# Kernel optimization log

Measured on AMD Instinct MI355X. Metric: run time of the kernel, lower is better.

The kernel has to match this reference:

```python
import jax, jax.numpy as jnp
import numpy as np
from jax import lax

IMG_H, IMG_W = 800.0, 800.0
REG_WEIGHTS = (10.0, 10.0, 5.0, 5.0)
SCORE_THRESH = 0.05
NMS_THRESH = 0.5
NUM_DETECTIONS = 100
MIN_SIZE = 1.0
BBOX_XFORM_CLIP = float(np.log(1000.0 / 16.0))


def setup_inputs() -> dict:
    key = jax.random.key(0)
    k1, k2, k3, k4 = jax.random.split(key, 4)
    N, C = 1000, 81
    class_logit = jax.random.normal(k1, (N, C), dtype=jnp.float32) * 2.0
    box_regression = jax.random.normal(k2, (N, C * 4), dtype=jnp.float32)
    # proposals: valid (x1,y1,x2,y2) boxes inside the 800x800 image
    ctr = jax.random.uniform(k3, (N, 2), dtype=jnp.float32) * 800.0
    wh = jax.random.uniform(k4, (N, 2), dtype=jnp.float32) * 200.0 + 8.0
    x1y1 = jnp.clip(ctr - 0.5 * wh, 0.0, 800.0)
    x2y2 = jnp.clip(ctr + 0.5 * wh, 0.0, 800.0)
    proposal = jnp.concatenate([x1y1, x2y2], axis=1)
    return dict(class_logit=class_logit, box_regression=box_regression, proposal=proposal)


def decode_boxes(deltas, boxes):
    # deltas: [..., 4] (dx,dy,dw,dh); boxes: [..., 4] (x1,y1,x2,y2)
    wx, wy, ww, wh = REG_WEIGHTS
    widths = boxes[..., 2] - boxes[..., 0]
    heights = boxes[..., 3] - boxes[..., 1]
    ctr_x = boxes[..., 0] + 0.5 * widths
    ctr_y = boxes[..., 1] + 0.5 * heights
    dx = deltas[..., 0] / wx
    dy = deltas[..., 1] / wy
    dw = jnp.minimum(deltas[..., 2] / ww, BBOX_XFORM_CLIP)
    dh = jnp.minimum(deltas[..., 3] / wh, BBOX_XFORM_CLIP)
    pcx = dx * widths + ctr_x
    pcy = dy * heights + ctr_y
    pw = jnp.exp(dw) * widths
    ph = jnp.exp(dh) * heights
    return jnp.stack([pcx - 0.5 * pw, pcy - 0.5 * ph, pcx + 0.5 * pw, pcy + 0.5 * ph], axis=-1)


def pairwise_iou(b):
    # b: [N, 4] -> [N, N]
    area = (b[:, 2] - b[:, 0]) * (b[:, 3] - b[:, 1])
    lt = jnp.maximum(b[:, None, :2], b[None, :, :2])
    rb = jnp.minimum(b[:, None, 2:], b[None, :, 2:])
    wh = jnp.clip(rb - lt, 0.0)
    inter = wh[..., 0] * wh[..., 1]
    return inter / (area[:, None] + area[None, :] - inter + 1e-9)


def nms_one_class(boxes, scores):
    # boxes: [N, 4]; scores: [N] with invalid entries masked to -1.
    # Exact greedy NMS: sort by score desc, suppress IoU > NMS_THRESH.
    N = boxes.shape[0]
    order = jnp.argsort(-scores)
    b = boxes[order]
    s = scores[order]
    iou = pairwise_iou(b)
    valid = s > -0.5

    def body(carry, xs):
        keep, i = carry
        row, v = xs
        suppressed = jnp.any(keep & (row > NMS_THRESH))
        keep = keep.at[i].set(v & jnp.logical_not(suppressed))
        return (keep, i + 1), None

    (keep, _), _ = lax.scan(body, (jnp.zeros((N,), bool), jnp.int32(0)), (iou, valid))
    s_kept = jnp.where(keep, s, -1.0)
    top_s, top_i = lax.top_k(s_kept, NUM_DETECTIONS)  # kept are already score-sorted
    out_valid = top_s > -0.5
    out_boxes = jnp.where(out_valid[:, None], b[top_i], 0.0)
    out_scores = jnp.where(out_valid, top_s, 0.0)
    return out_boxes, out_scores, out_valid


def reference(class_logit, box_regression, proposal):
    N, C = class_logit.shape
    pred_score = jax.nn.softmax(class_logit, axis=-1)           # [N, C]
    deltas = box_regression.reshape(N, C, 4)
    boxes = decode_boxes(deltas[:, 1:, :], proposal[:, None, :])  # [N, C-1, 4]
    # clip to image (process_box)
    boxes = jnp.stack([
        jnp.clip(boxes[..., 0], 0.0, IMG_W),
        jnp.clip(boxes[..., 1], 0.0, IMG_H),
        jnp.clip(boxes[..., 2], 0.0, IMG_W),
        jnp.clip(boxes[..., 3], 0.0, IMG_H),
    ], axis=-1)
    w = boxes[..., 2] - boxes[..., 0]
    h = boxes[..., 3] - boxes[..., 1]
    score_fg = pred_score[:, 1:]                                 # [N, C-1]
    valid = (score_fg >= SCORE_THRESH) & (w >= MIN_SIZE) & (h >= MIN_SIZE)
    scores_m = jnp.where(valid, score_fg, -1.0)
    boxes_c = jnp.transpose(boxes, (1, 0, 2))                    # [C-1, N, 4]
    scores_c = scores_m.T                                        # [C-1, N]
    out_boxes, out_scores, out_valid = jax.vmap(nms_one_class)(boxes_c, scores_c)
    labels = jnp.broadcast_to(jnp.arange(1, C, dtype=jnp.int32)[:, None], out_scores.shape)
    labels = jnp.where(out_valid, labels, 0)
    # padded per-class detections: boxes [C-1, D, 4], scores/labels/valid [C-1, D]
    return out_boxes, out_scores, labels, out_valid
```

## Files before the change

kernel.cpp:

```cpp
#include <hip/hip_runtime.h>
#include <math.h>

#define N_PROP   1000
#define C_ALL    81
#define N_FG     80
#define TOPK     100
#define CAP      1024
#define IMG_WH   800.0f
#define SCORE_TH 0.05f
#define NMS_TH   0.5f
#define MIN_SZ   1.0f
#define BBOX_CLIP 4.135166556742356f

#define DEC_BLK  320
#define NMS_BLK  256

typedef unsigned long long u64;

#define WS_CNT_STRIDE 16
#define WS_KEYS_OFF   8192
#define WS_FLT_OFF    (WS_KEYS_OFF + N_FG * CAP * 8)
#define WS_REQUIRED   (WS_FLT_OFF + 5ull * N_FG * CAP * 4)

__global__ __launch_bounds__(DEC_BLK) void decode_kernel(
    const float* __restrict__ logits,
    const float* __restrict__ boxreg,
    const float* __restrict__ prop,
    char* __restrict__ ws)
{
    int*   cnt  = (int*)ws;
    u64*   wkey = (u64*)(ws + WS_KEYS_OFF);
    float* wx1  = (float*)(ws + WS_FLT_OFF);
    float* wy1  = wx1 + N_FG * CAP;
    float* wx2  = wy1 + N_FG * CAP;
    float* wy2  = wx2 + N_FG * CAP;
    float* war  = wy2 + N_FG * CAP;

    __shared__ float2 s_ms[4];

    const int b    = blockIdx.x;
    const int tid  = threadIdx.x;
    const int wave = tid >> 6;
    const int lane = tid & 63;

    if (wave < 4) {
        const float* row = logits + (4 * b + wave) * C_ALL;
        float v1 = row[lane];
        float v2 = (lane < C_ALL - 64) ? row[64 + lane] : 0.f;

        float m = (lane < C_ALL - 64) ? fmaxf(v1, v2) : v1;
        #pragma unroll
        for (int off = 32; off >= 1; off >>= 1)
            m = fmaxf(m, __shfl_xor(m, off, 64));

        float s = expf(v1 - m) + ((lane < C_ALL - 64) ? expf(v2 - m) : 0.0f);
        #pragma unroll
        for (int off = 32; off >= 1; off >>= 1)
            s += __shfl_xor(s, off, 64);

        if (lane == 0) s_ms[wave] = make_float2(m, s);
    }
    __syncthreads();

    const int r   = tid / N_FG;
    const int cc  = tid - r * N_FG;
    const int n   = 4 * b + r;
    const int col = cc + 1;

    float2 ms = s_ms[r];
    float score = expf(logits[n * C_ALL + col] - ms.x) / ms.y;

    float4 p = *(const float4*)(prop + n * 4);
    float w  = p.z - p.x;
    float h  = p.w - p.y;
    float pcx0 = p.x + 0.5f * w;
    float pcy0 = p.y + 0.5f * h;

    float4 d = *(const float4*)(boxreg + n * (C_ALL * 4) + col * 4);
    float dx = d.x / 10.0f;
    float dy = d.y / 10.0f;
    float dw = fminf(d.z / 5.0f, BBOX_CLIP);
    float dh = fminf(d.w / 5.0f, BBOX_CLIP);

    float pcx = dx * w + pcx0;
    float pcy = dy * h + pcy0;
    float pw  = expf(dw) * w;
    float ph  = expf(dh) * h;

    float x1 = fminf(fmaxf(pcx - 0.5f * pw, 0.0f), IMG_WH);
    float y1 = fminf(fmaxf(pcy - 0.5f * ph, 0.0f), IMG_WH);
    float x2 = fminf(fmaxf(pcx + 0.5f * pw, 0.0f), IMG_WH);
    float y2 = fminf(fmaxf(pcy + 0.5f * ph, 0.0f), IMG_WH);

    float bw = x2 - x1;
    float bh = y2 - y1;
    if (score >= SCORE_TH && bw >= MIN_SZ && bh >= MIN_SZ) {
        int slot = atomicAdd(&cnt[cc * WS_CNT_STRIDE], 1);
        unsigned int fb = __float_as_uint(score);
        int base = cc * CAP + slot;
        wkey[base] = ((u64)fb << 10) | (u64)(1023 - n);
        wx1[base] = x1; wy1[base] = y1; wx2[base] = x2; wy2[base] = y2;
        war[base] = bw * bh;
    }
}

__global__ __launch_bounds__(NMS_BLK) void nms_kernel(
    const char* __restrict__ ws,
    float* __restrict__ out)
{
    const int*   cnt  = (const int*)ws;
    const u64*   wkey = (const u64*)(ws + WS_KEYS_OFF);
    const float* wx1  = (const float*)(ws + WS_FLT_OFF);
    const float* wy1  = wx1 + N_FG * CAP;
    const float* wx2  = wy1 + N_FG * CAP;
    const float* wy2  = wx2 + N_FG * CAP;
    const float* war  = wy2 + N_FG * CAP;

    __shared__ u64   s_key[CAP];
    __shared__ float cx1[CAP], cy1[CAP], cx2[CAP], cy2[CAP], car[CAP];
    __shared__ u64   s_skey[CAP];
    __shared__ float sx1[CAP], sy1[CAP], sx2[CAP], sy2[CAP], sar[CAP];
    __shared__ u64   s_mask[256 * 4];
    __shared__ u64   s_keep[4];
    __shared__ unsigned char s_rem[CAP];
    __shared__ int   s_emit;

    const int c   = blockIdx.x;
    const int tid = threadIdx.x;
    const int col = c + 1;

    const int OFF_SCORES = N_FG * TOPK * 4;
    const int OFF_LABELS = OFF_SCORES + N_FG * TOPK;
    const int OFF_VALID  = OFF_LABELS + N_FG * TOPK;

    if (tid < 175) {
        float4 z = make_float4(0.f, 0.f, 0.f, 0.f);
        if (tid < 100)      ((float4*)(out + c * TOPK * 4))[tid] = z;
        else if (tid < 125) ((float4*)(out + OFF_SCORES + c * TOPK))[tid - 100] = z;
        else if (tid < 150) ((float4*)(out + OFF_LABELS + c * TOPK))[tid - 125] = z;
        else                ((float4*)(out + OFF_VALID  + c * TOPK))[tid - 150] = z;
    }
    if (tid == 0) s_emit = 0;

    const int V = cnt[c * WS_CNT_STRIDE];
    if (V == 0) return;

    for (int t = tid; t < V; t += NMS_BLK) {
        int base = c * CAP + t;
        s_key[t] = wkey[base];
        cx1[t] = wx1[base]; cy1[t] = wy1[base];
        cx2[t] = wx2[base]; cy2[t] = wy2[base];
        car[t] = war[base];
    }
    __syncthreads();

    for (int t = tid; t < V; t += NMS_BLK) {
        u64 myk = s_key[t];
        int rank = 0;
        #pragma unroll 4
        for (int j = 0; j < V; ++j) rank += (s_key[j] > myk) ? 1 : 0;
        s_skey[rank] = myk;
        sx1[rank] = cx1[t]; sy1[rank] = cy1[t];
        sx2[rank] = cx2[t]; sy2[rank] = cy2[t];
        sar[rank] = car[t];
    }
    __syncthreads();

    if (V <= 64) {
        if (tid < 64) {
            const int lane = tid;
            bool act = lane < V;
            float bx1 = 0.f, by1 = 0.f, bx2 = 0.f, by2 = 0.f, bar = 0.f;
            if (act) {
                bx1 = sx1[lane]; by1 = sy1[lane];
                bx2 = sx2[lane]; by2 = sy2[lane];
                bar = sar[lane];
            }
            u64 myrow = 0;
            for (int i = 0; i < V; ++i) {
                float ix1 = __shfl(bx1, i, 64);
                float iy1 = __shfl(by1, i, 64);
                float ix2 = __shfl(bx2, i, 64);
                float iy2 = __shfl(by2, i, 64);
                float iar = __shfl(bar, i, 64);
                float lx = fmaxf(ix1, bx1);
                float ly = fmaxf(iy1, by1);
                float rx = fminf(ix2, bx2);
                float ry = fminf(iy2, by2);
                float iw = fmaxf(rx - lx, 0.0f);
                float ih = fmaxf(ry - ly, 0.0f);
                float inter = iw * ih;
                float iou = inter / (iar + bar - inter + 1e-9f);
                u64 bal = __ballot(act && (iou > NMS_TH));
                if (lane == i) {
                    u64 upper = (i == 63) ? 0ull : ~((1ull << (i + 1)) - 1ull);
                    myrow = bal & upper;
                }
            }
            u64 S = 0, K = 0;
            for (int i = 0; i < V; ++i) {
                if (!((S >> i) & 1ull)) {
                    K |= 1ull << i;
                    S |= __shfl(myrow, i, 64);
                }
            }
            if (act && ((K >> lane) & 1ull)) {
                int rank = __popcll(K & ((1ull << lane) - 1ull));
                float score = __uint_as_float((unsigned int)(s_skey[lane] >> 10));
                out[(c * TOPK + rank) * 4 + 0] = bx1;
                out[(c * TOPK + rank) * 4 + 1] = by1;
                out[(c * TOPK + rank) * 4 + 2] = bx2;
                out[(c * TOPK + rank) * 4 + 3] = by2;
                out[OFF_SCORES + c * TOPK + rank] = score;
                out[OFF_LABELS + c * TOPK + rank] = (float)col;
                out[OFF_VALID  + c * TOPK + rank] = 1.0f;
            }
        }
    } else if (V <= 256) {
        for (int i = tid; i < V; i += NMS_BLK) {
            float x1i = sx1[i], y1i = sy1[i], x2i = sx2[i], y2i = sy2[i];
            float ai  = sar[i];
            for (int w = 0; w < 4; ++w) {
                u64 mrow = 0;
                int j0 = w << 6;
                int j1 = min(V, j0 + 64);
                for (int j = max(j0, i + 1); j < j1; ++j) {
                    float lx = fmaxf(x1i, sx1[j]);
                    float ly = fmaxf(y1i, sy1[j]);
                    float rx = fminf(x2i, sx2[j]);
                    float ry = fminf(y2i, sy2[j]);
                    float iw = fmaxf(rx - lx, 0.0f);
                    float ih = fmaxf(ry - ly, 0.0f);
                    float inter = iw * ih;
                    float iou = inter / (ai + sar[j] - inter + 1e-9f);
                    if (iou > NMS_TH) mrow |= 1ull << (j - j0);
                }
                s_mask[(i << 2) + w] = mrow;
            }
        }
        __syncthreads();

        if (tid == 0) {
            u64 r0 = 0, r1 = 0, r2 = 0, r3 = 0;
            u64 k0 = 0, k1 = 0, k2 = 0, k3 = 0;
            int kept = 0;
            u64 p0 = s_mask[0], p1 = s_mask[1], p2 = s_mask[2], p3 = s_mask[3];
            u64 q0 = 0, q1 = 0, q2 = 0, q3 = 0;
            if (V > 1) {
                const u64* nr = &s_mask[4];
                q0 = nr[0]; q1 = nr[1]; q2 = nr[2]; q3 = nr[3];
            }
            for (int i = 0; i < V; ++i) {
                u64 t0 = 0, t1 = 0, t2 = 0, t3 = 0;
                if (i + 2 < V) {
                    const u64* nr = &s_mask[(i + 2) << 2];
                    t0 = nr[0]; t1 = nr[1]; t2 = nr[2]; t3 = nr[3];
                }
                int w = i >> 6;
                u64 bit = 1ull << (i & 63);
                u64 rw = (w == 0) ? r0 : (w == 1) ? r1 : (w == 2) ? r2 : r3;
                if (!(rw & bit)) {
                    if (w == 0) k0 |= bit; else if (w == 1) k1 |= bit;
                    else if (w == 2) k2 |= bit; else k3 |= bit;
                    if (++kept >= TOPK) break;
                    r0 |= p0; r1 |= p1; r2 |= p2; r3 |= p3;
                }
                p0 = q0; p1 = q1; p2 = q2; p3 = q3;
                q0 = t0; q1 = t1; q2 = t2; q3 = t3;
            }
            s_keep[0] = k0; s_keep[1] = k1; s_keep[2] = k2; s_keep[3] = k3;
        }
        __syncthreads();

        u64 kw0 = s_keep[0], kw1 = s_keep[1], kw2 = s_keep[2], kw3 = s_keep[3];
        for (int t = tid; t < V; t += NMS_BLK) {
            int w = t >> 6;
            u64 kw = (w == 0) ? kw0 : (w == 1) ? kw1 : (w == 2) ? kw2 : kw3;
            if (!((kw >> (t & 63)) & 1ull)) continue;
            int rank = 0;
            if (w > 0) rank += __popcll(kw0);
            if (w > 1) rank += __popcll(kw1);
            if (w > 2) rank += __popcll(kw2);
            rank += __popcll(kw & ((1ull << (t & 63)) - 1ull));
            if (rank < TOPK) {
                float score = __uint_as_float((unsigned int)(s_skey[t] >> 10));
                out[(c * TOPK + rank) * 4 + 0] = sx1[t];
                out[(c * TOPK + rank) * 4 + 1] = sy1[t];
                out[(c * TOPK + rank) * 4 + 2] = sx2[t];
                out[(c * TOPK + rank) * 4 + 3] = sy2[t];
                out[OFF_SCORES + c * TOPK + rank] = score;
                out[OFF_LABELS + c * TOPK + rank] = (float)col;
                out[OFF_VALID  + c * TOPK + rank] = 1.0f;
            }
        }
    } else {
        for (int t = tid; t < V; t += NMS_BLK) s_rem[t] = 0;
        __syncthreads();
        for (int i = 0; i < V; ++i) {
            if (s_rem[i]) continue;
            if (tid == 0) {
                int k = s_emit;
                if (k < TOPK) {
                    float score = __uint_as_float((unsigned int)(s_skey[i] >> 10));
                    out[(c * TOPK + k) * 4 + 0] = sx1[i];
                    out[(c * TOPK + k) * 4 + 1] = sy1[i];
                    out[(c * TOPK + k) * 4 + 2] = sx2[i];
                    out[(c * TOPK + k) * 4 + 3] = sy2[i];
                    out[OFF_SCORES + c * TOPK + k] = score;
                    out[OFF_LABELS + c * TOPK + k] = (float)col;
                    out[OFF_VALID  + c * TOPK + k] = 1.0f;
                }
                s_emit = k + 1;
            }
            float x1i = sx1[i], y1i = sy1[i], x2i = sx2[i], y2i = sy2[i];
            float ai  = sar[i];
            for (int jj = i + 1 + tid; jj < V; jj += NMS_BLK) {
                if (s_rem[jj]) continue;
                float lx = fmaxf(x1i, sx1[jj]);
                float ly = fmaxf(y1i, sy1[jj]);
                float rx = fminf(x2i, sx2[jj]);
                float ry = fminf(y2i, sy2[jj]);
                float iw = fmaxf(rx - lx, 0.0f);
                float ih = fmaxf(ry - ly, 0.0f);
                float inter = iw * ih;
                float iou = inter / (ai + sar[jj] - inter + 1e-9f);
                if (iou > NMS_TH) s_rem[jj] = 1;
            }
            __syncthreads();
            if (s_emit >= TOPK) break;
        }
    }
}

__global__ __launch_bounds__(512) void roihead_fused_kernel(
    const float* __restrict__ logits,
    const float* __restrict__ boxreg,
    const float* __restrict__ prop,
    float* __restrict__ out)
{
    __shared__ float2 s_stats[N_PROP];
    __shared__ u64   s_key[CAP];
    __shared__ float cx1[CAP], cy1[CAP], cx2[CAP], cy2[CAP], car[CAP];
    __shared__ u64   s_skey[CAP];
    __shared__ float sx1[CAP], sy1[CAP], sx2[CAP], sy2[CAP], sar[CAP];
    __shared__ u64   s_mask[256 * 4];
    __shared__ u64   s_keep[4];
    __shared__ unsigned char s_rem[CAP];
    __shared__ int   s_cnt, s_emit;

    const int c   = blockIdx.x;
    const int tid = threadIdx.x;
    const int col = c + 1;

    const int OFF_SCORES = N_FG * TOPK * 4;
    const int OFF_LABELS = OFF_SCORES + N_FG * TOPK;
    const int OFF_VALID  = OFF_LABELS + N_FG * TOPK;

    if (tid < 175) {
        float4 z = make_float4(0.f, 0.f, 0.f, 0.f);
        if (tid < 100)      ((float4*)(out + c * TOPK * 4))[tid] = z;
        else if (tid < 125) ((float4*)(out + OFF_SCORES + c * TOPK))[tid - 100] = z;
        else if (tid < 150) ((float4*)(out + OFF_LABELS + c * TOPK))[tid - 125] = z;
        else                ((float4*)(out + OFF_VALID  + c * TOPK))[tid - 150] = z;
    }
    if (tid == 0) { s_cnt = 0; s_emit = 0; }

    for (int n = tid; n < N_PROP; n += 512) {
        const float* row = logits + n * C_ALL;
        float m = -1e30f;
        for (int j = 0; j < C_ALL; ++j) m = fmaxf(m, row[j]);
        float s = 0.0f;
        for (int j = 0; j < C_ALL; ++j) s += expf(row[j] - m);
        s_stats[n] = make_float2(m, s);
    }
    __syncthreads();

    for (int n = tid; n < N_PROP; n += 512) {
        float2 ms = s_stats[n];
        float score = expf(logits[n * C_ALL + col] - ms.x) / ms.y;
        float4 p = *(const float4*)(prop + n * 4);
        float w  = p.z - p.x;
        float h  = p.w - p.y;
        float pcx0 = p.x + 0.5f * w;
        float pcy0 = p.y + 0.5f * h;
        float4 d = *(const float4*)(boxreg + n * (C_ALL * 4) + col * 4);
        float dx = d.x / 10.0f;
        float dy = d.y / 10.0f;
        float dw = fminf(d.z / 5.0f, BBOX_CLIP);
        float dh = fminf(d.w / 5.0f, BBOX_CLIP);
        float pcx = dx * w + pcx0;
        float pcy = dy * h + pcy0;
        float pw  = expf(dw) * w;
        float ph  = expf(dh) * h;
        float x1 = fminf(fmaxf(pcx - 0.5f * pw, 0.0f), IMG_WH);
        float y1 = fminf(fmaxf(pcy - 0.5f * ph, 0.0f), IMG_WH);
        float x2 = fminf(fmaxf(pcx + 0.5f * pw, 0.0f), IMG_WH);
        float y2 = fminf(fmaxf(pcy + 0.5f * ph, 0.0f), IMG_WH);
        float bw = x2 - x1;
        float bh = y2 - y1;
        if (score >= SCORE_TH && bw >= MIN_SZ && bh >= MIN_SZ) {
            int slot = atomicAdd(&s_cnt, 1);
            unsigned int fb = __float_as_uint(score);
            s_key[slot] = ((u64)fb << 20) | ((u64)(1023 - n) << 10) | (u64)slot;
            cx1[slot] = x1; cy1[slot] = y1; cx2[slot] = x2; cy2[slot] = y2;
            car[slot] = bw * bh;
        }
    }
    __syncthreads();

    const int V = s_cnt;
    if (V == 0) return;

    for (int t = tid; t < V; t += 512) {
        u64 myk = s_key[t];
        int rank = 0;
        for (int j = 0; j < V; ++j) rank += (s_key[j] > myk) ? 1 : 0;
        s_skey[rank] = myk;
        sx1[rank] = cx1[t]; sy1[rank] = cy1[t];
        sx2[rank] = cx2[t]; sy2[rank] = cy2[t];
        sar[rank] = car[t];
    }
    __syncthreads();

    if (V <= 64) {
        if (tid < 64) {
            const int lane = tid;
            bool act = lane < V;
            float bx1 = 0.f, by1 = 0.f, bx2 = 0.f, by2 = 0.f, bar = 0.f;
            if (act) {
                bx1 = sx1[lane]; by1 = sy1[lane];
                bx2 = sx2[lane]; by2 = sy2[lane];
                bar = sar[lane];
            }
            u64 myrow = 0;
            for (int i = 0; i < V; ++i) {
                float ix1 = __shfl(bx1, i, 64);
                float iy1 = __shfl(by1, i, 64);
                float ix2 = __shfl(bx2, i, 64);
                float iy2 = __shfl(by2, i, 64);
                float iar = __shfl(bar, i, 64);
                float lx = fmaxf(ix1, bx1);
                float ly = fmaxf(iy1, by1);
                float rx = fminf(ix2, bx2);
                float ry = fminf(iy2, by2);
                float iw = fmaxf(rx - lx, 0.0f);
                float ih = fmaxf(ry - ly, 0.0f);
                float inter = iw * ih;
                float iou = inter / (iar + bar - inter + 1e-9f);
                u64 bal = __ballot(act && (iou > NMS_TH));
                if (lane == i) {
                    u64 upper = (i == 63) ? 0ull : ~((1ull << (i + 1)) - 1ull);
                    myrow = bal & upper;
                }
            }
            u64 S = 0, K = 0;
            for (int i = 0; i < V; ++i) {
                if (!((S >> i) & 1ull)) {
                    K |= 1ull << i;
                    S |= __shfl(myrow, i, 64);
                }
            }
            if (act && ((K >> lane) & 1ull)) {
                int rank = __popcll(K & ((1ull << lane) - 1ull));
                float score = __uint_as_float((unsigned int)(s_skey[lane] >> 20));
                out[(c * TOPK + rank) * 4 + 0] = bx1;
                out[(c * TOPK + rank) * 4 + 1] = by1;
                out[(c * TOPK + rank) * 4 + 2] = bx2;
                out[(c * TOPK + rank) * 4 + 3] = by2;
                out[OFF_SCORES + c * TOPK + rank] = score;
                out[OFF_LABELS + c * TOPK + rank] = (float)col;
                out[OFF_VALID  + c * TOPK + rank] = 1.0f;
            }
        }
    } else if (V <= 256) {
        for (int i = tid; i < V; i += 512) {
            float x1i = sx1[i], y1i = sy1[i], x2i = sx2[i], y2i = sy2[i];
            float ai  = sar[i];
            for (int w = 0; w < 4; ++w) {
                u64 mrow = 0;
                int j0 = w << 6;
                int j1 = min(V, j0 + 64);
                for (int j = max(j0, i + 1); j < j1; ++j) {
                    float lx = fmaxf(x1i, sx1[j]);
                    float ly = fmaxf(y1i, sy1[j]);
                    float rx = fminf(x2i, sx2[j]);
                    float ry = fminf(y2i, sy2[j]);
                    float iw = fmaxf(rx - lx, 0.0f);
                    float ih = fmaxf(ry - ly, 0.0f);
                    float inter = iw * ih;
                    float iou = inter / (ai + sar[j] - inter + 1e-9f);
                    if (iou > NMS_TH) mrow |= 1ull << (j - j0);
                }
                s_mask[(i << 2) + w] = mrow;
            }
        }
        __syncthreads();
        if (tid == 0) {
            u64 r0 = 0, r1 = 0, r2 = 0, r3 = 0;
            u64 k0 = 0, k1 = 0, k2 = 0, k3 = 0;
            int kept = 0;
            for (int i = 0; i < V; ++i) {
                int w = i >> 6;
                u64 bit = 1ull << (i & 63);
                u64 rw = (w == 0) ? r0 : (w == 1) ? r1 : (w == 2) ? r2 : r3;
                if (rw & bit) continue;
                if (w == 0) k0 |= bit; else if (w == 1) k1 |= bit;
                else if (w == 2) k2 |= bit; else k3 |= bit;
                if (++kept >= TOPK) break;
                const u64* mr = &s_mask[i << 2];
                r0 |= mr[0]; r1 |= mr[1]; r2 |= mr[2]; r3 |= mr[3];
            }
            s_keep[0] = k0; s_keep[1] = k1; s_keep[2] = k2; s_keep[3] = k3;
        }
        __syncthreads();
        u64 kw0 = s_keep[0], kw1 = s_keep[1], kw2 = s_keep[2], kw3 = s_keep[3];
        for (int t = tid; t < V; t += 512) {
            int w = t >> 6;
            u64 kw = (w == 0) ? kw0 : (w == 1) ? kw1 : (w == 2) ? kw2 : kw3;
            if (!((kw >> (t & 63)) & 1ull)) continue;
            int rank = 0;
            if (w > 0) rank += __popcll(kw0);
            if (w > 1) rank += __popcll(kw1);
            if (w > 2) rank += __popcll(kw2);
            rank += __popcll(kw & ((1ull << (t & 63)) - 1ull));
            if (rank < TOPK) {
                float score = __uint_as_float((unsigned int)(s_skey[t] >> 20));
                out[(c * TOPK + rank) * 4 + 0] = sx1[t];
                out[(c * TOPK + rank) * 4 + 1] = sy1[t];
                out[(c * TOPK + rank) * 4 + 2] = sx2[t];
                out[(c * TOPK + rank) * 4 + 3] = sy2[t];
                out[OFF_SCORES + c * TOPK + rank] = score;
                out[OFF_LABELS + c * TOPK + rank] = (float)col;
                out[OFF_VALID  + c * TOPK + rank] = 1.0f;
            }
        }
    } else {
        for (int t = tid; t < V; t += 512) s_rem[t] = 0;
        __syncthreads();
        for (int i = 0; i < V; ++i) {
            if (s_rem[i]) continue;
            if (tid == 0) {
                int k = s_emit;
                if (k < TOPK) {
                    float score = __uint_as_float((unsigned int)(s_skey[i] >> 20));
                    out[(c * TOPK + k) * 4 + 0] = sx1[i];
                    out[(c * TOPK + k) * 4 + 1] = sy1[i];
                    out[(c * TOPK + k) * 4 + 2] = sx2[i];
                    out[(c * TOPK + k) * 4 + 3] = sy2[i];
                    out[OFF_SCORES + c * TOPK + k] = score;
                    out[OFF_LABELS + c * TOPK + k] = (float)col;
                    out[OFF_VALID  + c * TOPK + k] = 1.0f;
                }
                s_emit = k + 1;
            }
            float x1i = sx1[i], y1i = sy1[i], x2i = sx2[i], y2i = sy2[i];
            float ai  = sar[i];
            for (int jj = i + 1 + tid; jj < V; jj += 512) {
                if (s_rem[jj]) continue;
                float lx = fmaxf(x1i, sx1[jj]);
                float ly = fmaxf(y1i, sy1[jj]);
                float rx = fminf(x2i, sx2[jj]);
                float ry = fminf(y2i, sy2[jj]);
                float iw = fmaxf(rx - lx, 0.0f);
                float ih = fmaxf(ry - ly, 0.0f);
                float inter = iw * ih;
                float iou = inter / (ai + sar[jj] - inter + 1e-9f);
                if (iou > NMS_TH) s_rem[jj] = 1;
            }
            __syncthreads();
            if (s_emit >= TOPK) break;
        }
    }
}

extern "C" void kernel_launch(void* const* d_in, const int* in_sizes, int n_in,
                              void* d_out, int out_size, void* d_ws, size_t ws_size,
                              hipStream_t stream) {
    const float* class_logit = (const float*)d_in[0];
    const float* box_reg     = (const float*)d_in[1];
    const float* proposal    = (const float*)d_in[2];
    float* out = (float*)d_out;

    if (ws_size >= WS_REQUIRED) {
        hipMemsetAsync(d_ws, 0, N_FG * WS_CNT_STRIDE * sizeof(int), stream);
        decode_kernel<<<N_PROP / 4, DEC_BLK, 0, stream>>>(
            class_logit, box_reg, proposal, (char*)d_ws);
        nms_kernel<<<N_FG, NMS_BLK, 0, stream>>>((const char*)d_ws, out);
    } else {
        roihead_fused_kernel<<<N_FG, 512, 0, stream>>>(
            class_logit, box_reg, proposal, out);
    }
}
```

Measured before the change: 84.96 us.

## Replace global atomic compaction with dense workspace and in-block ballot compaction

The decode kernel now writes every (class, proposal) box and a masked score densely into the workspace instead of compacting valid candidates through global atomics. Each NMS block scans all 1000 entries for its class and compacts the valid ones into shared memory using wave ballots and a shared-memory atomic. This removes the memset launch and the contended global atomics. In exchange, each NMS block reads the full dense per-class slab and does a serial 4-iteration scan before the sort. Candidate order within shared memory now depends on the order in which waves claim slots, but the rank sort on keys should make the result deterministic.

```diff
diff --git a/kernel.cpp b/kernel.cpp
--- a/kernel.cpp
+++ b/kernel.cpp
@@ -17,10 +17,8 @@
 
 typedef unsigned long long u64;
 
-#define WS_CNT_STRIDE 16
-#define WS_KEYS_OFF   8192
-#define WS_FLT_OFF    (WS_KEYS_OFF + N_FG * CAP * 8)
-#define WS_REQUIRED   (WS_FLT_OFF + 5ull * N_FG * CAP * 4)
+#define WS_SCORE_OFF  (N_FG * CAP * 16)
+#define WS_REQUIRED   (WS_SCORE_OFF + (size_t)N_FG * CAP * 4)
 
 __global__ __launch_bounds__(DEC_BLK) void decode_kernel(
     const float* __restrict__ logits,
@@ -28,13 +26,8 @@
     const float* __restrict__ prop,
     char* __restrict__ ws)
 {
-    int*   cnt  = (int*)ws;
-    u64*   wkey = (u64*)(ws + WS_KEYS_OFF);
-    float* wx1  = (float*)(ws + WS_FLT_OFF);
-    float* wy1  = wx1 + N_FG * CAP;
-    float* wx2  = wy1 + N_FG * CAP;
-    float* wy2  = wx2 + N_FG * CAP;
-    float* war  = wy2 + N_FG * CAP;
+    float4* wbox   = (float4*)ws;
+    float*  wscore = (float*)(ws + WS_SCORE_OFF);
 
     __shared__ float2 s_ms[4];
 
@@ -62,8 +55,8 @@
     }
     __syncthreads();
 
-    const int r   = tid / N_FG;
-    const int cc  = tid - r * N_FG;
+    const int cc  = tid >> 2;
+    const int r   = tid & 3;
     const int n   = 4 * b + r;
     const int col = cc + 1;
 
@@ -94,27 +87,19 @@
 
     float bw = x2 - x1;
     float bh = y2 - y1;
-    if (score >= SCORE_TH && bw >= MIN_SZ && bh >= MIN_SZ) {
-        int slot = atomicAdd(&cnt[cc * WS_CNT_STRIDE], 1);
-        unsigned int fb = __float_as_uint(score);
-        int base = cc * CAP + slot;
-        wkey[base] = ((u64)fb << 10) | (u64)(1023 - n);
-        wx1[base] = x1; wy1[base] = y1; wx2[base] = x2; wy2[base] = y2;
-        war[base] = bw * bh;
-    }
+    bool ok = (score >= SCORE_TH) && (bw >= MIN_SZ) && (bh >= MIN_SZ);
+
+    int base = cc * CAP + n;
+    wbox[base]   = make_float4(x1, y1, x2, y2);
+    wscore[base] = ok ? score : 0.0f;
 }
 
 __global__ __launch_bounds__(NMS_BLK) void nms_kernel(
     const char* __restrict__ ws,
     float* __restrict__ out)
 {
-    const int*   cnt  = (const int*)ws;
-    const u64*   wkey = (const u64*)(ws + WS_KEYS_OFF);
-    const float* wx1  = (const float*)(ws + WS_FLT_OFF);
-    const float* wy1  = wx1 + N_FG * CAP;
-    const float* wx2  = wy1 + N_FG * CAP;
-    const float* wy2  = wx2 + N_FG * CAP;
-    const float* war  = wy2 + N_FG * CAP;
+    const float4* wbox   = (const float4*)ws;
+    const float*  wscore = (const float*)(ws + WS_SCORE_OFF);
 
     __shared__ u64   s_key[CAP];
     __shared__ float cx1[CAP], cy1[CAP], cx2[CAP], cy2[CAP], car[CAP];
@@ -123,11 +108,12 @@
     __shared__ u64   s_mask[256 * 4];
     __shared__ u64   s_keep[4];
     __shared__ unsigned char s_rem[CAP];
-    __shared__ int   s_emit;
-
-    const int c   = blockIdx.x;
-    const int tid = threadIdx.x;
-    const int col = c + 1;
+    __shared__ int   s_cnt, s_emit;
+
+    const int c    = blockIdx.x;
+    const int tid  = threadIdx.x;
+    const int lane = tid & 63;
+    const int col  = c + 1;
 
     const int OFF_SCORES = N_FG * TOPK * 4;
     const int OFF_LABELS = OFF_SCORES + N_FG * TOPK;
@@ -140,19 +126,32 @@
         else if (tid < 150) ((float4*)(out + OFF_LABELS + c * TOPK))[tid - 125] = z;
         else                ((float4*)(out + OFF_VALID  + c * TOPK))[tid - 150] = z;
     }
-    if (tid == 0) s_emit = 0;
-
-    const int V = cnt[c * WS_CNT_STRIDE];
+    if (tid == 0) { s_cnt = 0; s_emit = 0; }
+    __syncthreads();
+
+    for (int t0 = 0; t0 < N_PROP; t0 += NMS_BLK) {
+        int t = t0 + tid;
+        float sc = (t < N_PROP) ? wscore[c * CAP + t] : 0.0f;
+        float4 bx = (t < N_PROP) ? wbox[c * CAP + t]
+                                 : make_float4(0.f, 0.f, 0.f, 0.f);
+        bool valid = sc > 0.0f;
+        u64 bal = __ballot(valid);
+        int pop = __popcll(bal);
+        int wbase = 0;
+        if (lane == 0) wbase = atomicAdd(&s_cnt, pop);
+        wbase = __shfl(wbase, 0, 64);
+        if (valid) {
+            int slot = wbase + __popcll(bal & ((1ull << lane) - 1ull));
+            s_key[slot] = ((u64)__float_as_uint(sc) << 10) | (u64)(1023 - t);
+            cx1[slot] = bx.x; cy1[slot] = bx.y;
+            cx2[slot] = bx.z; cy2[slot] = bx.w;
+            car[slot] = (bx.z - bx.x) * (bx.w - bx.y);
+        }
+    }
+    __syncthreads();
+
+    const int V = s_cnt;
     if (V == 0) return;
-
-    for (int t = tid; t < V; t += NMS_BLK) {
-        int base = c * CAP + t;
-        s_key[t] = wkey[base];
-        cx1[t] = wx1[base]; cy1[t] = wy1[base];
-        cx2[t] = wx2[base]; cy2[t] = wy2[base];
-        car[t] = war[base];
-    }
-    __syncthreads();
 
     for (int t = tid; t < V; t += NMS_BLK) {
         u64 myk = s_key[t];
@@ -168,7 +167,6 @@
 
     if (V <= 64) {
         if (tid < 64) {
-            const int lane = tid;
             bool act = lane < V;
             float bx1 = 0.f, by1 = 0.f, bx2 = 0.f, by2 = 0.f, bar = 0.f;
             if (act) {
@@ -582,7 +580,6 @@
     float* out = (float*)d_out;
 
     if (ws_size >= WS_REQUIRED) {
-        hipMemsetAsync(d_ws, 0, N_FG * WS_CNT_STRIDE * sizeof(int), stream);
         decode_kernel<<<N_PROP / 4, DEC_BLK, 0, stream>>>(
             class_logit, box_reg, proposal, (char*)d_ws);
         nms_kernel<<<N_FG, NMS_BLK, 0, stream>>>((const char*)d_ws, out);
```

Measured after the change: 86.00 us. Within noise of the previous version (+1.2%).
